# Kernel optimization log

Measured on AMD Instinct MI355X. Metric: run time of the kernel, lower is better.

Reference implementation:

```python
import jax, jax.numpy as jnp
import numpy as np

N = 100000      # nodes
E = 1600000     # edges (before self-loops)
IN = 128        # in_channels
H = 8           # heads (layer 0)
C = 8           # hidden_node_channels_per_head
OUT = 64        # out_channels (layer 1, single head, concat=False)
NEG_SLOPE = 0.2 # PyG GATConv LeakyReLU slope


def setup_inputs() -> dict:
    key = jax.random.key(0)
    ks = jax.random.split(key, 10)
    x = jax.random.normal(ks[0], (N, IN), jnp.float32)
    edge_index = jax.random.randint(ks[1], (2, E), 0, N, dtype=jnp.int32)
    s0 = 1.0 / np.sqrt(IN)
    s1 = 1.0 / np.sqrt(H * C)
    return {
        "x": x,
        "edge_index": edge_index,
        "W0": jax.random.normal(ks[2], (IN, H * C), jnp.float32) * s0,
        "att_src0": jax.random.normal(ks[3], (H, C), jnp.float32) * s1,
        "att_dst0": jax.random.normal(ks[4], (H, C), jnp.float32) * s1,
        "b0": jnp.zeros((H * C,), jnp.float32),
        "W1": jax.random.normal(ks[5], (H * C, OUT), jnp.float32) * s1,
        "att_src1": jax.random.normal(ks[6], (1, OUT), jnp.float32) * s1,
        "att_dst1": jax.random.normal(ks[7], (1, OUT), jnp.float32) * s1,
        "b1": jnp.zeros((OUT,), jnp.float32),
    }


def _gat_conv(x, src, dst, W, a_src, a_dst, b, heads, ch, concat):
    # x: [N, F_in]; src/dst: [E'] (self-loops included)
    xW = (x @ W).reshape(N, heads, ch)                     # [N, H, C]
    a_s = jnp.einsum('nhc,hc->nh', xW, a_src)              # [N, H]
    a_d = jnp.einsum('nhc,hc->nh', xW, a_dst)              # [N, H]
    e = jax.nn.leaky_relu(a_s[src] + a_d[dst], NEG_SLOPE)  # [E', H]
    # segment softmax over incoming edges of each dst node
    m = jax.ops.segment_max(e, dst, num_segments=N)        # [N, H]
    ex = jnp.exp(e - m[dst])
    denom = jax.ops.segment_sum(ex, dst, num_segments=N)   # [N, H]
    alpha = ex / denom[dst]                                # [E', H]
    out = jax.ops.segment_sum(alpha[:, :, None] * xW[src], dst, num_segments=N)  # [N, H, C]
    if concat:
        return out.reshape(N, heads * ch) + b
    return out.mean(axis=1) + b


def reference(x, edge_index, W0, att_src0, att_dst0, b0, W1, att_src1, att_dst1, b1):
    src, dst = edge_index[0], edge_index[1]
    loops = jnp.arange(N, dtype=src.dtype)                 # PyG add_self_loops=True
    src = jnp.concatenate([src, loops])
    dst = jnp.concatenate([dst, loops])
    # layer 0: GATConv(IN -> C per head, H heads, concat) ; ELU (dropout = identity at eval)
    h = jax.nn.elu(_gat_conv(x, src, dst, W0, att_src0, att_dst0, b0, H, C, True))
    # layer 1: GATConv(H*C -> OUT, 1 head, concat=False) ; ELU
    out = jax.nn.elu(_gat_conv(h, src, dst, W1, att_src1, att_dst1, b1, 1, OUT, False))
    return out
```

## Files before the change

kernel.cpp:

```cpp
#include <hip/hip_runtime.h>
#include <hip/hip_fp16.h>
#include <math.h>


#define CAPS 12
#define STRIDE 12
#define NBMAX 512
#define SLOTS 6144
#define OVF   1024
#define REGION 7168
#define LOG2E 1.44269504f

typedef _Float16 h2_t  __attribute__((ext_vector_type(2)));
typedef _Float16 h8_t  __attribute__((ext_vector_type(8)));
typedef float    f4_t  __attribute__((ext_vector_type(4)));
typedef unsigned int u4_t __attribute__((ext_vector_type(4)));

__device__ __forceinline__ float lrelu(float v) { return v >= 0.f ? v : 0.2f * v; }
__device__ __forceinline__ float eluf(float v)  {
    return v > 0.f ? v : __builtin_amdgcn_exp2f(v * LOG2E) - 1.f;
}

#define MIX_LO(acc, pk, w) asm("v_fma_mix_f32 %0, %1, %2, %0 op_sel:[0,0,0] op_sel_hi:[1,0,0]" : "+v"(acc) : "v"(pk), "v"(w))
#define MIX_HI(acc, pk, w) asm("v_fma_mix_f32 %0, %1, %2, %0 op_sel:[1,0,0] op_sel_hi:[1,0,0]" : "+v"(acc) : "v"(pk), "v"(w))

__device__ __forceinline__ void gemm_body(
    int gb, const float* __restrict__ x, int N,
    __half* __restrict__ xw, __half* __restrict__ as, __half* __restrict__ ad,
    h8_t* Bl)
{
    int wave = threadIdx.x >> 6, lane = threadIdx.x & 63;
    int row0 = gb * 128 + wave * 16;
    if (row0 >= N) return;
    int quad = lane >> 4, c16 = lane & 15;
    int myrow = min(row0 + c16, N - 1);
    const float* xr = x + (size_t)myrow * 128;
    h8_t a[4];
    #pragma unroll
    for (int ks = 0; ks < 4; ks++) {
        int kb = ks * 32 + quad * 8;
        float4 v0 = *(const float4*)(xr + kb);
        float4 v1 = *(const float4*)(xr + kb + 4);
        h8_t av;
        av[0] = (_Float16)v0.x; av[1] = (_Float16)v0.y;
        av[2] = (_Float16)v0.z; av[3] = (_Float16)v0.w;
        av[4] = (_Float16)v1.x; av[5] = (_Float16)v1.y;
        av[6] = (_Float16)v1.z; av[7] = (_Float16)v1.w;
        a[ks] = av;
    }
    int rbase = row0 + quad * 4;
    #pragma unroll
    for (int ct = 0; ct < 5; ct++) {
        f4_t acc = {0.f, 0.f, 0.f, 0.f};
        #pragma unroll
        for (int ks = 0; ks < 4; ks++) {
            h8_t b = Bl[(ct * 4 + ks) * 64 + lane];
            acc = __builtin_amdgcn_mfma_f32_16x16x32_f16(a[ks], b, acc, 0, 0, 0);
        }
        if (ct < 4) {
            int col = ct * 16 + c16;
            #pragma unroll
            for (int r = 0; r < 4; r++) {
                int row = rbase + r;
                if (row < N) xw[(size_t)row * 64 + col] = __float2half(acc[r]);
            }
        } else {
            #pragma unroll
            for (int r = 0; r < 4; r++) {
                int row = rbase + r;
                if (row < N) {
                    float sc = acc[r] * LOG2E;
                    if (c16 < 8) as[(size_t)row * 8 + c16] = __float2half(sc);
                    else         ad[(size_t)row * 8 + (c16 - 8)] = __float2half(sc);
                }
            }
        }
    }
}

__global__ __launch_bounds__(512, 4) void kGB(
    const float* __restrict__ x, const float* __restrict__ W0,
    const float* __restrict__ aS0, const float* __restrict__ aD0, int N,
    __half* __restrict__ xw, __half* __restrict__ as, __half* __restrict__ ad,
    int gemmBlocks,
    const int* __restrict__ src, const int* __restrict__ dst, int E, int perBlock,
    unsigned* __restrict__ bucketBuf, int* __restrict__ gcur, int* __restrict__ cntT,
    int NB, int binBlocks)
{
    __shared__ __align__(16) char smem[NBMAX * STRIDE * 4 + NBMAX * 4];
    int b = blockIdx.x;
    int T = gemmBlocks + binBlocks;
    int lo = (int)((long long)b * gemmBlocks / T);
    int hi = (int)((long long)(b + 1) * gemmBlocks / T);
    if (hi > lo) {
        h8_t* Bl = (h8_t*)smem;
        for (int g = threadIdx.x; g < 1280; g += 512) {
            int col  = g & 15;
            int quad = (g >> 4) & 3;
            int ks   = (g >> 6) & 3;
            int ct   = g >> 8;
            h8_t av;
            if (ct < 4) {
                #pragma unroll
                for (int j = 0; j < 8; j++) {
                    int k = ks * 32 + quad * 8 + j;
                    av[j] = (_Float16)W0[k * 64 + ct * 16 + col];
                }
            } else {
                int h = col & 7;
                const float* att = (col < 8) ? aS0 : aD0;
                #pragma unroll
                for (int j = 0; j < 8; j++) {
                    int k = ks * 32 + quad * 8 + j;
                    float v = 0.f;
                    #pragma unroll
                    for (int cc = 0; cc < 8; cc++)
                        v += W0[k * 64 + h * 8 + cc] * att[h * 8 + cc];
                    av[j] = (_Float16)v;
                }
            }
            Bl[g] = av;
        }
        __syncthreads();
        gemm_body(lo, x, N, xw, as, ad, Bl);
    } else {
        int pb = b - hi;
        unsigned* stage = (unsigned*)smem;
        int* scnt = (int*)(smem + NBMAX * STRIDE * 4);
        int tid = threadIdx.x;
        for (int i = tid; i < NB; i += 512) scnt[i] = 0;
        __syncthreads();
        int e0 = pb * perBlock, e1 = min(E, e0 + perBlock);
        for (int i = e0 + tid; i < e1; i += 512) {
            int d2 = dst[i], s2 = src[i];
            int bk = d2 >> 8;
            unsigned rec = ((unsigned)(d2 & 255) << 22) | (unsigned)s2;
            int pos = atomicAdd(&scnt[bk], 1);
            if (pos < CAPS) {
                stage[bk * STRIDE + pos] = rec;
            } else {
                int g = atomicAdd(&gcur[bk], 1);
                if (g < OVF) bucketBuf[(size_t)bk * REGION + SLOTS + g] = rec;
            }
        }
        __syncthreads();
        const uint4* stv = (const uint4*)stage;
        for (int t = tid; t < NB; t += 512) {
            int n = min(scnt[t], CAPS);
            cntT[(size_t)pb * NBMAX + t] = n;
            uint4* gp = (uint4*)&bucketBuf[(size_t)t * REGION + (size_t)pb * CAPS];
            gp[0] = stv[t * 3 + 0];
            gp[1] = stv[t * 3 + 1];
            gp[2] = stv[t * 3 + 2];
        }
    }
}

__global__ __launch_bounds__(256) void kP2(
    const unsigned* __restrict__ bucketBuf, const int* __restrict__ gcur,
    const int* __restrict__ cntT, int NB, int N,
    int* __restrict__ rowS, int* __restrict__ rowE, int* __restrict__ adj)
{
    __shared__ int cnts[512];
    __shared__ int deg[256];
    __shared__ int curl[256];
    __shared__ int sc[256];
    int b = blockIdx.x, tid = threadIdx.x;
    int lo = b << 8;
    int hi = min(N, lo + 256);
    int cnt = hi - lo;
    for (int i = tid; i < 512; i += 256) cnts[i] = cntT[(size_t)i * NBMAX + b];
    deg[tid] = 0;
    __syncthreads();
    const unsigned* buf = bucketBuf + (size_t)b * REGION;
    for (int blk = tid; blk < 512; blk += 256) {
        int c = cnts[blk];
        const unsigned* p = buf + blk * CAPS;
        for (int i2 = 0; i2 < c; i2++) atomicAdd(&deg[p[i2] >> 22], 1);
    }
    int ovf = min(gcur[b], OVF);
    for (int e = tid; e < ovf; e += 256) atomicAdd(&deg[buf[SLOTS + e] >> 22], 1);
    __syncthreads();
    int d = deg[tid];
    sc[tid] = d;
    __syncthreads();
    for (int off2 = 1; off2 < 256; off2 <<= 1) {
        int xv = (tid >= off2) ? sc[tid - off2] : 0;
        __syncthreads();
        sc[tid] += xv;
        __syncthreads();
    }
    int base = b * REGION;
    int o = (tid ? sc[tid - 1] : 0);
    curl[tid] = base + o;
    if (tid < cnt) { rowS[lo + tid] = base + o; rowE[lo + tid] = base + o + d; }
    __syncthreads();
    for (int blk = tid; blk < 512; blk += 256) {
        int c = cnts[blk];
        const unsigned* p = buf + blk * CAPS;
        for (int i2 = 0; i2 < c; i2++) {
            unsigned r = p[i2];
            int pp = atomicAdd(&curl[r >> 22], 1);
            adj[pp] = (int)(r & 0x3FFFFF);
        }
    }
    for (int e = tid; e < ovf; e += 256) {
        unsigned r = buf[SLOTS + e];
        int pp = atomicAdd(&curl[r >> 22], 1);
        adj[pp] = (int)(r & 0x3FFFFF);
    }
}

__global__ __launch_bounds__(512) void k_agg8(
    const __half* __restrict__ xw, const __half* __restrict__ as, const __half* __restrict__ ad,
    const int* __restrict__ rowS, const int* __restrict__ rowE, const int* __restrict__ adj,
    const float* __restrict__ bias,
    const float* __restrict__ W1, const float* __restrict__ aS1, const float* __restrict__ aD1,
    int N, __half* __restrict__ hw, float* __restrict__ as1, float* __restrict__ ad1)
{
    __shared__ __align__(16) h8_t Wl[512];
    __shared__ __align__(16) h8_t hst[32][9];
    __shared__ float psum[4][32];
    __shared__ float pdsum[4][32];
    {
        int g = threadIdx.x;
        int col  = g & 15;
        int quad = (g >> 4) & 3;
        int ks   = (g >> 6) & 1;
        int ct   = g >> 7;
        h8_t av;
        #pragma unroll
        for (int j = 0; j < 8; j++) {
            int k = ks * 32 + quad * 8 + j;
            av[j] = (_Float16)W1[k * 64 + ct * 16 + col];
        }
        Wl[g] = av;
    }
    int n = (blockIdx.x * 512 + threadIdx.x) >> 4;
    int sub  = threadIdx.x & 15;
    bool active = n < N;
    int e2 = sub >> 3;
    int hh = sub & 7;
    int rs = active ? rowS[n] : 0;
    int re = active ? rowE[n] : 0;
    const u4_t* xwv = (const u4_t*)xw;
    unsigned nc = active ? (unsigned)n : 0u;
    float adv = __half2float(ad[nc * 8u + hh]);
    float shift = lrelu(__half2float(as[nc * 8u + hh]) + adv);
    float accv[8];
    #pragma unroll
    for (int k = 0; k < 8; k++) accv[k] = 0.f;
    float dsum = 0.f;

    int j = rs;
    bool vA0 = j + e2 < re,     vB0 = j + 2 + e2 < re;
    int  sA0 = adj[(unsigned)(vA0 ? j + e2 : 0)];
    int  sB0 = adj[(unsigned)(vB0 ? j + 2 + e2 : 0)];
    bool vA1 = j + 4 + e2 < re, vB1 = j + 6 + e2 < re;
    int  sA1 = adj[(unsigned)(vA1 ? j + 4 + e2 : 0)];
    int  sB1 = adj[(unsigned)(vB1 ? j + 6 + e2 : 0)];
    float eA0 = lrelu(__half2float(as[(unsigned)sA0 * 8u + hh]) + adv);
    float eB0 = lrelu(__half2float(as[(unsigned)sB0 * 8u + hh]) + adv);
    u4_t xA0 = xwv[(unsigned)sA0 * 8u + hh];
    u4_t xB0 = xwv[(unsigned)sB0 * 8u + hh];
    float eA1, eB1; u4_t xA1, xB1;

    for (;;) {
        {
            bool vA2 = j + 8 + e2 < re, vB2 = j + 10 + e2 < re;
            int nsA = adj[(unsigned)(vA2 ? j + 8 + e2 : 0)];
            int nsB = adj[(unsigned)(vB2 ? j + 10 + e2 : 0)];
            eA1 = lrelu(__half2float(as[(unsigned)sA1 * 8u + hh]) + adv);
            eB1 = lrelu(__half2float(as[(unsigned)sB1 * 8u + hh]) + adv);
            xA1 = xwv[(unsigned)sA1 * 8u + hh];
            xB1 = xwv[(unsigned)sB1 * 8u + hh];
            float wA = vA0 ? __builtin_amdgcn_exp2f(eA0 - shift) : 0.f;
            float wB = vB0 ? __builtin_amdgcn_exp2f(eB0 - shift) : 0.f;
            dsum += wA + wB;
            #pragma unroll
            for (int q = 0; q < 4; q++) {
                MIX_LO(accv[2 * q],     xA0[q], wA);
                MIX_HI(accv[2 * q + 1], xA0[q], wA);
            }
            #pragma unroll
            for (int q = 0; q < 4; q++) {
                MIX_LO(accv[2 * q],     xB0[q], wB);
                MIX_HI(accv[2 * q + 1], xB0[q], wB);
            }
            vA0 = vA2; vB0 = vB2; sA0 = nsA; sB0 = nsB;
        }
        j += 4;
        if (!__any(vA1)) break;
        {
            bool vA2 = j + 8 + e2 < re, vB2 = j + 10 + e2 < re;
            int nsA = adj[(unsigned)(vA2 ? j + 8 + e2 : 0)];
            int nsB = adj[(unsigned)(vB2 ? j + 10 + e2 : 0)];
            eA0 = lrelu(__half2float(as[(unsigned)sA0 * 8u + hh]) + adv);
            eB0 = lrelu(__half2float(as[(unsigned)sB0 * 8u + hh]) + adv);
            xA0 = xwv[(unsigned)sA0 * 8u + hh];
            xB0 = xwv[(unsigned)sB0 * 8u + hh];
            float wA = vA1 ? __builtin_amdgcn_exp2f(eA1 - shift) : 0.f;
            float wB = vB1 ? __builtin_amdgcn_exp2f(eB1 - shift) : 0.f;
            dsum += wA + wB;
            #pragma unroll
            for (int q = 0; q < 4; q++) {
                MIX_LO(accv[2 * q],     xA1[q], wA);
                MIX_HI(accv[2 * q + 1], xA1[q], wA);
            }
            #pragma unroll
            for (int q = 0; q < 4; q++) {
                MIX_LO(accv[2 * q],     xB1[q], wB);
                MIX_HI(accv[2 * q + 1], xB1[q], wB);
            }
            vA1 = vA2; vB1 = vB2; sA1 = nsA; sB1 = nsB;
        }
        j += 4;
        if (!__any(vA0)) break;
    }
    #pragma unroll
    for (int k = 0; k < 8; k++) accv[k] += __shfl_xor(accv[k], 8, 64);
    dsum += __shfl_xor(dsum, 8, 64);
    if (e2 == 0) {
        int nl = (threadIdx.x >> 4);
        h8_t o;
        if (active) {
            float inv = 1.f / (1.f + dsum);
            h8_t sv = *(const h8_t*)(xw + (size_t)n * 64 + hh * 8);
            float4 b0 = *(const float4*)(bias + hh * 8);
            float4 b1 = *(const float4*)(bias + hh * 8 + 4);
            float bb[8] = {b0.x, b0.y, b0.z, b0.w, b1.x, b1.y, b1.z, b1.w};
            #pragma unroll
            for (int k = 0; k < 8; k++) {
                float v = (accv[k] + (float)sv[k]) * inv + bb[k];
                o[k] = (_Float16)eluf(v);
            }
        } else {
            #pragma unroll
            for (int k = 0; k < 8; k++) o[k] = (_Float16)0.f;
        }
        hst[nl][hh] = o;
    }
    __syncthreads();
    {
        int wave = threadIdx.x >> 6, lane = threadIdx.x & 63;
        int ct   = wave >> 1;
        int half = wave & 1;
        int quad = lane >> 4, c16 = lane & 15;
        int lrow = half * 16 + c16;
        int row0 = blockIdx.x * 32 + half * 16;
        h8_t a0 = hst[lrow][quad];
        h8_t a1 = hst[lrow][4 + quad];
        int rbase = row0 + quad * 4;
        f4_t acc = {0.f, 0.f, 0.f, 0.f};
        acc = __builtin_amdgcn_mfma_f32_16x16x32_f16(a0, Wl[(ct * 2 + 0) * 64 + lane], acc, 0, 0, 0);
        acc = __builtin_amdgcn_mfma_f32_16x16x32_f16(a1, Wl[(ct * 2 + 1) * 64 + lane], acc, 0, 0, 0);
        float s1c = aS1[ct * 16 + c16];
        float d1c = aD1[ct * 16 + c16];
        int col = ct * 16 + c16;
        float ps[4], pd[4];
        #pragma unroll
        for (int r = 0; r < 4; r++) {
            int rr = rbase + r;
            if (rr < N) hw[(size_t)rr * 64 + col] = __float2half(acc[r]);
            ps[r] = acc[r] * s1c;
            pd[r] = acc[r] * d1c;
        }
        #pragma unroll
        for (int r = 0; r < 4; r++) {
            #pragma unroll
            for (int off = 1; off < 16; off <<= 1) {
                ps[r] += __shfl_xor(ps[r], off, 64);
                pd[r] += __shfl_xor(pd[r], off, 64);
            }
        }
        if (c16 == 0) {
            #pragma unroll
            for (int r = 0; r < 4; r++) {
                int lr = half * 16 + quad * 4 + r;
                psum[ct][lr]  = ps[r];
                pdsum[ct][lr] = pd[r];
            }
        }
    }
    __syncthreads();
    if (threadIdx.x < 32) {
        int lr = threadIdx.x;
        int rr = blockIdx.x * 32 + lr;
        if (rr < N) {
            float s  = psum[0][lr] + psum[1][lr] + psum[2][lr] + psum[3][lr];
            float dd = pdsum[0][lr] + pdsum[1][lr] + pdsum[2][lr] + pdsum[3][lr];
            as1[rr] = s * LOG2E;
            ad1[rr] = dd * LOG2E;
        }
    }
}

__global__ __launch_bounds__(512) void k_agg1(
    const __half* __restrict__ hw, const float* __restrict__ as, const float* __restrict__ ad,
    const int* __restrict__ rowS, const int* __restrict__ rowE, const int* __restrict__ adj,
    const float* __restrict__ bias, int N, float* __restrict__ outp)
{
    int n = (blockIdx.x * 512 + threadIdx.x) >> 4;
    int sub  = threadIdx.x & 15;
    if (n >= N) return;
    int e2 = sub >> 3;
    int hh = sub & 7;
    int rs = rowS[n], re = rowE[n];
    const u4_t* hwv = (const u4_t*)hw;
    float adv = ad[n];
    float shift = lrelu(as[n] + adv);
    float accv[8];
    #pragma unroll
    for (int k = 0; k < 8; k++) accv[k] = 0.f;
    float dsum = 0.f;

    int j = rs;
    bool vA0 = j + e2 < re,     vB0 = j + 2 + e2 < re;
    int  sA0 = adj[(unsigned)(vA0 ? j + e2 : 0)];
    int  sB0 = adj[(unsigned)(vB0 ? j + 2 + e2 : 0)];
    bool vA1 = j + 4 + e2 < re, vB1 = j + 6 + e2 < re;
    int  sA1 = adj[(unsigned)(vA1 ? j + 4 + e2 : 0)];
    int  sB1 = adj[(unsigned)(vB1 ? j + 6 + e2 : 0)];
    float eA0 = lrelu(as[(unsigned)sA0] + adv);
    float eB0 = lrelu(as[(unsigned)sB0] + adv);
    u4_t xA0 = hwv[(unsigned)sA0 * 8u + hh];
    u4_t xB0 = hwv[(unsigned)sB0 * 8u + hh];
    float eA1, eB1; u4_t xA1, xB1;

    for (;;) {
        {
            bool vA2 = j + 8 + e2 < re, vB2 = j + 10 + e2 < re;
            int nsA = adj[(unsigned)(vA2 ? j + 8 + e2 : 0)];
            int nsB = adj[(unsigned)(vB2 ? j + 10 + e2 : 0)];
            eA1 = lrelu(as[(unsigned)sA1] + adv);
            eB1 = lrelu(as[(unsigned)sB1] + adv);
            xA1 = hwv[(unsigned)sA1 * 8u + hh];
            xB1 = hwv[(unsigned)sB1 * 8u + hh];
            float wA = vA0 ? __builtin_amdgcn_exp2f(eA0 - shift) : 0.f;
            float wB = vB0 ? __builtin_amdgcn_exp2f(eB0 - shift) : 0.f;
            dsum += wA + wB;
            #pragma unroll
            for (int q = 0; q < 4; q++) {
                MIX_LO(accv[2 * q],     xA0[q], wA);
                MIX_HI(accv[2 * q + 1], xA0[q], wA);
            }
            #pragma unroll
            for (int q = 0; q < 4; q++) {
                MIX_LO(accv[2 * q],     xB0[q], wB);
                MIX_HI(accv[2 * q + 1], xB0[q], wB);
            }
            vA0 = vA2; vB0 = vB2; sA0 = nsA; sB0 = nsB;
        }
        j += 4;
        if (!__any(vA1)) break;
        {
            bool vA2 = j + 8 + e2 < re, vB2 = j + 10 + e2 < re;
            int nsA = adj[(unsigned)(vA2 ? j + 8 + e2 : 0)];
            int nsB = adj[(unsigned)(vB2 ? j + 10 + e2 : 0)];
            eA0 = lrelu(as[(unsigned)sA0] + adv);
            eB0 = lrelu(as[(unsigned)sB0] + adv);
            xA0 = hwv[(unsigned)sA0 * 8u + hh];
            xB0 = hwv[(unsigned)sB0 * 8u + hh];
            float wA = vA1 ? __builtin_amdgcn_exp2f(eA1 - shift) : 0.f;
            float wB = vB1 ? __builtin_amdgcn_exp2f(eB1 - shift) : 0.f;
            dsum += wA + wB;
            #pragma unroll
            for (int q = 0; q < 4; q++) {
                MIX_LO(accv[2 * q],     xA1[q], wA);
                MIX_HI(accv[2 * q + 1], xA1[q], wA);
            }
            #pragma unroll
            for (int q = 0; q < 4; q++) {
                MIX_LO(accv[2 * q],     xB1[q], wB);
                MIX_HI(accv[2 * q + 1], xB1[q], wB);
            }
            vA1 = vA2; vB1 = vB2; sA1 = nsA; sB1 = nsB;
        }
        j += 4;
        if (!__any(vA0)) break;
    }
    #pragma unroll
    for (int k = 0; k < 8; k++) accv[k] += __shfl_xor(accv[k], 8, 64);
    dsum += __shfl_xor(dsum, 8, 64);
    if (e2 == 0) {
        float inv = 1.f / (1.f + dsum);
        h8_t sv = *(const h8_t*)(hw + (size_t)n * 64 + hh * 8);
        float4 b0 = *(const float4*)(bias + hh * 8);
        float4 b1 = *(const float4*)(bias + hh * 8 + 4);
        float bb[8] = {b0.x, b0.y, b0.z, b0.w, b1.x, b1.y, b1.z, b1.w};
        float ov[8];
        #pragma unroll
        for (int k = 0; k < 8; k++)
            ov[k] = eluf((accv[k] + (float)sv[k]) * inv + bb[k]);
        float4 o0 = {ov[0], ov[1], ov[2], ov[3]};
        float4 o1 = {ov[4], ov[5], ov[6], ov[7]};
        float4* op = (float4*)(outp + (size_t)n * 64 + hh * 8);
        op[0] = o0;
        op[1] = o1;
    }
}

extern "C" void kernel_launch(void* const* d_in, const int* in_sizes, int n_in,
                              void* d_out, int out_size, void* d_ws, size_t ws_size,
                              hipStream_t stream)
{
    const float* x   = (const float*)d_in[0];
    const int*   ei  = (const int*)d_in[1];
    const float* W0  = (const float*)d_in[2];
    const float* aS0 = (const float*)d_in[3];
    const float* aD0 = (const float*)d_in[4];
    const float* b0  = (const float*)d_in[5];
    const float* W1  = (const float*)d_in[6];
    const float* aS1 = (const float*)d_in[7];
    const float* aD1 = (const float*)d_in[8];
    const float* b1  = (const float*)d_in[9];

    const int N = in_sizes[0] / 128;
    const int E = in_sizes[1] / 2;
    const int* srcp = ei;
    const int* dstp = ei + E;

    const int NB  = (N + 255) >> 8;

    char* ws = (char*)d_ws;
    size_t off = 0;
    auto alloc = [&](size_t bytes) -> size_t {
        size_t o = off;
        off = (o + bytes + 255) & ~(size_t)255;
        return o;
    };
    __half* B1 = (__half*)(ws + alloc((size_t)N * 64 * 2));
    size_t b2Bytes = (size_t)N * 64 * 2;
    size_t bkBytes = (size_t)NB * REGION * 4;
    char*  region  = ws + alloc(b2Bytes > bkBytes ? b2Bytes : bkBytes);
    __half*   B2        = (__half*)region;
    unsigned* bucketBuf = (unsigned*)region;
    __half* as0 = (__half*)(ws + alloc((size_t)N * 8 * 2));
    __half* ad0 = (__half*)(ws + alloc((size_t)N * 8 * 2));
    float* as1 = (float*)(ws + alloc((size_t)N * 4));
    float* ad1 = (float*)(ws + alloc((size_t)N * 4));
    int*  rowS = (int*)(ws + alloc((size_t)(N + 1) * 4));
    int*  rowE = (int*)(ws + alloc((size_t)(N + 1) * 4));
    int*   adj = (int*)(ws + alloc((size_t)NB * REGION * 4));
    int*  gcur = (int*)(ws + alloc((size_t)NB * 4));
    int*  cntT = (int*)(ws + alloc((size_t)NBMAX * NBMAX * 4));

    const int gemmBlocks = (N + 127) / 128;
    const int binBlocks  = 512;
    const int perBlock   = (E + binBlocks - 1) / binBlocks;

    hipMemsetAsync(gcur, 0, (size_t)NB * 4, stream);
    kGB<<<gemmBlocks + binBlocks, 512, 0, stream>>>(
        x, W0, aS0, aD0, N, B1, as0, ad0, gemmBlocks,
        srcp, dstp, E, perBlock, bucketBuf, gcur, cntT, NB, binBlocks);
    kP2<<<NB, 256, 0, stream>>>(bucketBuf, gcur, cntT, NB, N, rowS, rowE, adj);

    const int agBlocks = (N + 31) / 32;
    k_agg8<<<agBlocks, 512, 0, stream>>>(B1, as0, ad0, rowS, rowE, adj, b0,
                                         W1, aS1, aD1, N, B2, as1, ad1);
    k_agg1<<<agBlocks, 512, 0, stream>>>(B2, as1, ad1, rowS, rowE, adj, b1, N, (float*)d_out);
}
```

Measured before the change: 232.1 us.

## Replace global overflow bucket with fixed per-block cells in edge binning

```diff
diff --git a/kernel.cpp b/kernel.cpp
--- a/kernel.cpp
+++ b/kernel.cpp
@@ -3,11 +3,10 @@
 #include <math.h>
 
 
-#define CAPS 12
-#define STRIDE 12
+#define CAPS 16
+#define CELL 48
 #define NBMAX 512
-#define SLOTS 6144
-#define OVF   1024
+#define BINB 256
 #define REGION 7168
 #define LOG2E 1.44269504f
 
@@ -84,10 +83,10 @@
     __half* __restrict__ xw, __half* __restrict__ as, __half* __restrict__ ad,
     int gemmBlocks,
     const int* __restrict__ src, const int* __restrict__ dst, int E, int perBlock,
-    unsigned* __restrict__ bucketBuf, int* __restrict__ gcur, int* __restrict__ cntT,
+    unsigned* __restrict__ bucketBuf, int* __restrict__ cntT,
     int NB, int binBlocks)
 {
-    __shared__ __align__(16) char smem[NBMAX * STRIDE * 4 + NBMAX * 4];
+    __shared__ __align__(16) char smem[NBMAX * CAPS * 4 + NBMAX * 4];
     int b = blockIdx.x;
     int T = gemmBlocks + binBlocks;
     int lo = (int)((long long)b * gemmBlocks / T);
@@ -126,7 +125,7 @@
     } else {
         int pb = b - hi;
         unsigned* stage = (unsigned*)smem;
-        int* scnt = (int*)(smem + NBMAX * STRIDE * 4);
+        int* scnt = (int*)(smem + NBMAX * CAPS * 4);
         int tid = threadIdx.x;
         for (int i = tid; i < NB; i += 512) scnt[i] = 0;
         __syncthreads();
@@ -137,77 +136,71 @@
             unsigned rec = ((unsigned)(d2 & 255) << 22) | (unsigned)s2;
             int pos = atomicAdd(&scnt[bk], 1);
             if (pos < CAPS) {
-                stage[bk * STRIDE + pos] = rec;
-            } else {
-                int g = atomicAdd(&gcur[bk], 1);
-                if (g < OVF) bucketBuf[(size_t)bk * REGION + SLOTS + g] = rec;
+                stage[bk * CAPS + pos] = rec;
+            } else if (pos < CELL) {
+                bucketBuf[((size_t)bk * BINB + pb) * CELL + pos] = rec;
             }
         }
         __syncthreads();
         const uint4* stv = (const uint4*)stage;
         for (int t = tid; t < NB; t += 512) {
-            int n = min(scnt[t], CAPS);
+            int n = min(scnt[t], CELL);
             cntT[(size_t)pb * NBMAX + t] = n;
-            uint4* gp = (uint4*)&bucketBuf[(size_t)t * REGION + (size_t)pb * CAPS];
-            gp[0] = stv[t * 3 + 0];
-            gp[1] = stv[t * 3 + 1];
-            gp[2] = stv[t * 3 + 2];
+            uint4* gp = (uint4*)&bucketBuf[((size_t)t * BINB + pb) * CELL];
+            gp[0] = stv[t * 4 + 0];
+            gp[1] = stv[t * 4 + 1];
+            gp[2] = stv[t * 4 + 2];
+            gp[3] = stv[t * 4 + 3];
         }
     }
 }
 
 __global__ __launch_bounds__(256) void kP2(
-    const unsigned* __restrict__ bucketBuf, const int* __restrict__ gcur,
-    const int* __restrict__ cntT, int NB, int N,
+    const unsigned* __restrict__ bucketBuf, const int* __restrict__ cntT,
+    int NB, int N,
     int* __restrict__ rowS, int* __restrict__ rowE, int* __restrict__ adj)
 {
-    __shared__ int cnts[512];
     __shared__ int deg[256];
     __shared__ int curl[256];
-    __shared__ int sc[256];
+    __shared__ int wsum[4];
     int b = blockIdx.x, tid = threadIdx.x;
     int lo = b << 8;
     int hi = min(N, lo + 256);
     int cnt = hi - lo;
-    for (int i = tid; i < 512; i += 256) cnts[i] = cntT[(size_t)i * NBMAX + b];
+    int myc = cntT[(size_t)tid * NBMAX + b];
     deg[tid] = 0;
     __syncthreads();
-    const unsigned* buf = bucketBuf + (size_t)b * REGION;
-    for (int blk = tid; blk < 512; blk += 256) {
-        int c = cnts[blk];
-        const unsigned* p = buf + blk * CAPS;
-        for (int i2 = 0; i2 < c; i2++) atomicAdd(&deg[p[i2] >> 22], 1);
-    }
-    int ovf = min(gcur[b], OVF);
-    for (int e = tid; e < ovf; e += 256) atomicAdd(&deg[buf[SLOTS + e] >> 22], 1);
+    const unsigned* buf = bucketBuf + (size_t)b * BINB * CELL;
+    {
+        const unsigned* p = buf + tid * CELL;
+        for (int i = 0; i < myc; i++) atomicAdd(&deg[p[i] >> 22], 1);
+    }
     __syncthreads();
     int d = deg[tid];
-    sc[tid] = d;
+    int lane = tid & 63, wid = tid >> 6;
+    int x = d;
+    #pragma unroll
+    for (int off = 1; off < 64; off <<= 1) {
+        int y = __shfl_up(x, off, 64);
+        if (lane >= off) x += y;
+    }
+    if (lane == 63) wsum[wid] = x;
     __syncthreads();
-    for (int off2 = 1; off2 < 256; off2 <<= 1) {
-        int xv = (tid >= off2) ? sc[tid - off2] : 0;
-        __syncthreads();
-        sc[tid] += xv;
-        __syncthreads();
-    }
+    int add = 0;
+    #pragma unroll
+    for (int w = 0; w < 4; w++) add += (w < wid) ? wsum[w] : 0;
+    int excl = x + add - d;
     int base = b * REGION;
-    int o = (tid ? sc[tid - 1] : 0);
-    curl[tid] = base + o;
-    if (tid < cnt) { rowS[lo + tid] = base + o; rowE[lo + tid] = base + o + d; }
+    curl[tid] = base + excl;
+    if (tid < cnt) { rowS[lo + tid] = base + excl; rowE[lo + tid] = base + excl + d; }
     __syncthreads();
-    for (int blk = tid; blk < 512; blk += 256) {
-        int c = cnts[blk];
-        const unsigned* p = buf + blk * CAPS;
-        for (int i2 = 0; i2 < c; i2++) {
-            unsigned r = p[i2];
+    {
+        const unsigned* p = buf + tid * CELL;
+        for (int i = 0; i < myc; i++) {
+            unsigned r = p[i];
             int pp = atomicAdd(&curl[r >> 22], 1);
             adj[pp] = (int)(r & 0x3FFFFF);
         }
-    }
-    for (int e = tid; e < ovf; e += 256) {
-        unsigned r = buf[SLOTS + e];
-        int pp = atomicAdd(&curl[r >> 22], 1);
-        adj[pp] = (int)(r & 0x3FFFFF);
     }
 }
 
@@ -531,7 +524,7 @@
     };
     __half* B1 = (__half*)(ws + alloc((size_t)N * 64 * 2));
     size_t b2Bytes = (size_t)N * 64 * 2;
-    size_t bkBytes = (size_t)NB * REGION * 4;
+    size_t bkBytes = (size_t)NB * BINB * CELL * 4;
     char*  region  = ws + alloc(b2Bytes > bkBytes ? b2Bytes : bkBytes);
     __half*   B2        = (__half*)region;
     unsigned* bucketBuf = (unsigned*)region;
@@ -542,18 +535,16 @@
     int*  rowS = (int*)(ws + alloc((size_t)(N + 1) * 4));
     int*  rowE = (int*)(ws + alloc((size_t)(N + 1) * 4));
     int*   adj = (int*)(ws + alloc((size_t)NB * REGION * 4));
-    int*  gcur = (int*)(ws + alloc((size_t)NB * 4));
-    int*  cntT = (int*)(ws + alloc((size_t)NBMAX * NBMAX * 4));
+    int*  cntT = (int*)(ws + alloc((size_t)BINB * NBMAX * 4));
 
     const int gemmBlocks = (N + 127) / 128;
-    const int binBlocks  = 512;
+    const int binBlocks  = BINB;
     const int perBlock   = (E + binBlocks - 1) / binBlocks;
 
-    hipMemsetAsync(gcur, 0, (size_t)NB * 4, stream);
     kGB<<<gemmBlocks + binBlocks, 512, 0, stream>>>(
         x, W0, aS0, aD0, N, B1, as0, ad0, gemmBlocks,
-        srcp, dstp, E, perBlock, bucketBuf, gcur, cntT, NB, binBlocks);
-    kP2<<<NB, 256, 0, stream>>>(bucketBuf, gcur, cntT, NB, N, rowS, rowE, adj);
+        srcp, dstp, E, perBlock, bucketBuf, cntT, NB, binBlocks);
+    kP2<<<NB, 256, 0, stream>>>(bucketBuf, cntT, NB, N, rowS, rowE, adj);
 
     const int agBlocks = (N + 31) / 32;
     k_agg8<<<agBlocks, 512, 0, stream>>>(B1, as0, ad0, rowS, rowE, adj, b0,
```

Result: faster. 224.0 us, median of 2 (-3.5%).
